# Kernel optimization log

Measured on AMD Instinct MI355X. Metric: run time of the kernel, lower is better.

## Reference

```python
import jax, jax.numpy as jnp
import numpy as np

V, D, H, L, FF, C = 32000, 512, 8, 3, 2048, 6
B, S = 32, 1024


def setup_inputs() -> dict:
    key = jax.random.key(0)
    ks = jax.random.split(key, 8)
    tokens = jax.random.randint(ks[0], (B, S), 0, V, dtype=jnp.int32)
    emb = jax.random.normal(ks[1], (V, D), dtype=jnp.float32) * 0.02
    qkv_w = jax.random.normal(ks[2], (L, D, 3 * D), dtype=jnp.float32) * (D ** -0.5)
    qkv_b = jnp.zeros((L, 3 * D), dtype=jnp.float32)
    fc_w = jax.random.normal(ks[3], (L, D, D), dtype=jnp.float32) * (D ** -0.5)
    fc_b = jnp.zeros((L, D), dtype=jnp.float32)
    gamma = jnp.ones((D,), dtype=jnp.float32)
    beta = jnp.zeros((D,), dtype=jnp.float32)
    fc1_w = jax.random.normal(ks[4], (D, FF), dtype=jnp.float32) * (D ** -0.5)
    fc1_b = jnp.zeros((FF,), dtype=jnp.float32)
    fc2_w = jax.random.normal(ks[5], (FF, C), dtype=jnp.float32) * (FF ** -0.5)
    fc2_b = jnp.zeros((C,), dtype=jnp.float32)
    return dict(tokens=tokens, emb=emb, qkv_w=qkv_w, qkv_b=qkv_b, fc_w=fc_w,
                fc_b=fc_b, gamma=gamma, beta=beta, fc1_w=fc1_w, fc1_b=fc1_b,
                fc2_w=fc2_w, fc2_b=fc2_b)


def _sinusoidal_pe(seq_len, dim):
    pos = jnp.arange(seq_len, dtype=jnp.float32)[:, None]
    div = jnp.exp(jnp.arange(0, dim, 2).astype(jnp.float32) * (-np.log(10000.0) / dim))
    pe = jnp.zeros((seq_len, dim), dtype=jnp.float32)
    pe = pe.at[:, 0::2].set(jnp.sin(pos * div))
    pe = pe.at[:, 1::2].set(jnp.cos(pos * div))
    return pe


def reference(tokens, emb, qkv_w, qkv_b, fc_w, fc_b, gamma, beta, fc1_w, fc1_b, fc2_w, fc2_b):
    b, s = tokens.shape
    dh = D // H
    scale = dh ** -0.5

    def layernorm(y):
        m = y.mean(-1, keepdims=True)
        v = ((y - m) ** 2).mean(-1, keepdims=True)
        return (y - m) * jax.lax.rsqrt(v + 1e-5) * gamma + beta

    x = emb[tokens] + _sinusoidal_pe(s, D)[None]  # [B,S,D]
    for l in range(L):
        qkv = (x @ qkv_w[l] + qkv_b[l]).reshape(b, s, H, 3, dh)
        q = qkv[..., 0, :].transpose(0, 2, 1, 3)  # [B,H,S,dh]
        k = qkv[..., 1, :].transpose(0, 2, 1, 3)
        v = qkv[..., 2, :].transpose(0, 2, 1, 3)
        attn = jax.nn.softmax(jnp.einsum('bhqd,bhkd->bhqk', q, k) * scale, axis=-1)
        o = jnp.einsum('bhqk,bhkd->bhqd', attn, v).transpose(0, 2, 1, 3).reshape(b, s, D)
        o = o @ fc_w[l] + fc_b[l]
        x = layernorm(o + x)
    pooled = x.mean(axis=1)  # [B,D]
    h = jax.nn.relu(pooled @ fc1_w + fc1_b)  # dropout is identity at inference
    return h @ fc2_w + fc2_b
```

## Files before the change

### kernel.cpp

```cpp
#include <hip/hip_runtime.h>
#include <cmath>

#define BS_TOK 32768
#define DMODEL 512
#define NHEAD 8
#define DHEAD 64
#define NLAYER 3
#define FFDIM 2048
#define NCLS 6
#define BATCH 32
#define SEQ 1024
#define QKVW 1536

typedef short short8 __attribute__((ext_vector_type(8)));
typedef float float4v __attribute__((ext_vector_type(4)));
#define MFMA_BF16 __builtin_amdgcn_mfma_f32_16x16x32_bf16
#define QSCALE 0.18033688011112042f

__device__ __forceinline__ unsigned short f2bf(float x) {
    return (unsigned short)((__float_as_uint(x) + 0x8000u) >> 16);
}

__global__ __launch_bounds__(128) void embed_pe_kernel(const int* __restrict__ tokens,
                                                       const float* __restrict__ emb,
                                                       float* __restrict__ X,
                                                       unsigned short* __restrict__ Xb) {
    int t = blockIdx.x;
    int pos = t & (SEQ - 1);
    int tok = tokens[t];
    int d0 = threadIdx.x * 4;
    float4 e = *(const float4*)(emb + (size_t)tok * DMODEL + d0);
    const float c = -9.210340371976184f / 512.0f;
    float div0 = expf((float)d0 * c);
    float div1 = expf((float)(d0 + 2) * c);
    float a0 = (float)pos * div0;
    float a1 = (float)pos * div1;
    e.x += sinf(a0); e.y += cosf(a0);
    e.z += sinf(a1); e.w += cosf(a1);
    *(float4*)(X + (size_t)t * DMODEL + d0) = e;
    *(ushort4*)(Xb + (size_t)t * DMODEL + d0) =
        make_ushort4(f2bf(e.x), f2bf(e.y), f2bf(e.z), f2bf(e.w));
}

__global__ __launch_bounds__(256) void transcvt_kernel(const float* __restrict__ in,
                                                       unsigned short* __restrict__ out,
                                                       int R, int C) {
    __shared__ float t[32][33];
    size_t base = (size_t)blockIdx.z * R * C;
    int c0 = blockIdx.x * 32, r0 = blockIdx.y * 32;
    int tx = threadIdx.x & 31, ty = threadIdx.x >> 5;
#pragma unroll
    for (int i = 0; i < 4; i++)
        t[ty + i * 8][tx] = in[base + (size_t)(r0 + ty + i * 8) * C + c0 + tx];
    __syncthreads();
#pragma unroll
    for (int i = 0; i < 4; i++)
        out[base + (size_t)(c0 + ty + i * 8) * R + r0 + tx] = f2bf(t[tx][ty + i * 8]);
}

__global__ __launch_bounds__(256) void transcvt_qkv_kernel(const float* __restrict__ in,
                                                           unsigned short* __restrict__ out) {
    __shared__ float t[32][33];
    int l = blockIdx.z;
    int n0 = blockIdx.x * 32, r0 = blockIdx.y * 32;
    int seg = n0 >> 9, nn = n0 & 511, h = nn >> 6, d0 = nn & 63;
    int c0 = h * 192 + seg * 64 + d0;
    float s = (seg == 0) ? QSCALE : 1.f;
    const float* inp = in + (size_t)l * DMODEL * QKVW;
    unsigned short* op = out + (size_t)l * QKVW * DMODEL;
    int tx = threadIdx.x & 31, ty = threadIdx.x >> 5;
#pragma unroll
    for (int i = 0; i < 4; i++)
        t[ty + i * 8][tx] = inp[(size_t)(r0 + ty + i * 8) * QKVW + c0 + tx];
    __syncthreads();
#pragma unroll
    for (int i = 0; i < 4; i++)
        op[(size_t)(n0 + ty + i * 8) * DMODEL + r0 + tx] = f2bf(t[tx][ty + i * 8] * s);
}

__global__ __launch_bounds__(256) void permbias_kernel(const float* __restrict__ qkv_b,
                                                       float* __restrict__ pb) {
    int i = blockIdx.x * 256 + threadIdx.x;
    int l = i / QKVW, n = i - l * QKVW;
    int seg = n >> 9, nn = n & 511, h = nn >> 6, d = nn & 63;
    float s = (seg == 0) ? QSCALE : 1.f;
    pb[i] = qkv_b[l * QKVW + h * 192 + seg * 64 + d] * s;
}

__global__ __launch_bounds__(256) void gemm_qkv_kernel(const unsigned short* __restrict__ A,
                                                       const unsigned short* __restrict__ Bt,
                                                       const float* __restrict__ pb,
                                                       unsigned short* __restrict__ QKc,
                                                       unsigned short* __restrict__ Vt,
                                                       int M) {
    __shared__ unsigned short As[128 * 40];
    __shared__ unsigned short Bs[128 * 40];
    int bm = blockIdx.y * 128, bn = blockIdx.x * 128;
    int tid = threadIdx.x;
    int w = tid >> 6, lane = tid & 63, l15 = lane & 15, quad = lane >> 4;
    int wm = (w & 1) * 64, wn = (w >> 1) * 64;

    float4v acc[4][4];
    float4v z = {0.f, 0.f, 0.f, 0.f};
#pragma unroll
    for (int i = 0; i < 4; i++)
#pragma unroll
        for (int j = 0; j < 4; j++) acc[i][j] = z;

    int r0 = tid >> 2, o0 = (tid & 3) * 8;
    int r1 = (tid + 256) >> 2, o1 = (tid & 3) * 8;

    for (int k0 = 0; k0 < DMODEL; k0 += 32) {
        __syncthreads();
        *(short8*)&As[r0 * 40 + o0] = *(const short8*)(A + (size_t)(bm + r0) * DMODEL + k0 + o0);
        *(short8*)&As[r1 * 40 + o1] = *(const short8*)(A + (size_t)(bm + r1) * DMODEL + k0 + o1);
        *(short8*)&Bs[r0 * 40 + o0] = *(const short8*)(Bt + (size_t)(bn + r0) * DMODEL + k0 + o0);
        *(short8*)&Bs[r1 * 40 + o1] = *(const short8*)(Bt + (size_t)(bn + r1) * DMODEL + k0 + o1);
        __syncthreads();
        short8 af[4], bf[4];
#pragma unroll
        for (int i = 0; i < 4; i++)
            af[i] = *(short8*)&As[(wm + i * 16 + l15) * 40 + quad * 8];
#pragma unroll
        for (int j = 0; j < 4; j++)
            bf[j] = *(short8*)&Bs[(wn + j * 16 + l15) * 40 + quad * 8];
#pragma unroll
        for (int i = 0; i < 4; i++)
#pragma unroll
            for (int j = 0; j < 4; j++)
                acc[i][j] = MFMA_BF16(af[i], bf[j], acc[i][j], 0, 0, 0);
    }

    float bj[4];
#pragma unroll
    for (int j = 0; j < 4; j++) bj[j] = pb[bn + wn + j * 16 + l15];

    if (bn < 1024) {
#pragma unroll
        for (int i = 0; i < 4; i++)
#pragma unroll
            for (int r = 0; r < 4; r++) {
                size_t row = (size_t)(bm + wm + i * 16 + quad * 4 + r);
#pragma unroll
                for (int j = 0; j < 4; j++)
                    QKc[row * 1024 + bn + wn + j * 16 + l15] = f2bf(acc[i][j][r] + bj[j]);
            }
    } else {
        int bl = bm >> 10;
        int sbase = (bm & 1023) + wm;
#pragma unroll
        for (int j = 0; j < 4; j++) {
            int colp = bn - 1024 + wn + j * 16 + l15;
            int h = colp >> 6, d = colp & 63;
            unsigned short* vb = Vt + ((size_t)(bl * 8 + h) * 64 + d) * 1024 + sbase;
#pragma unroll
            for (int i = 0; i < 4; i++) {
                ushort4 v4 = make_ushort4(f2bf(acc[i][j][0] + bj[j]),
                                          f2bf(acc[i][j][1] + bj[j]),
                                          f2bf(acc[i][j][2] + bj[j]),
                                          f2bf(acc[i][j][3] + bj[j]));
                *(ushort4*)(vb + i * 16 + quad * 4) = v4;
            }
        }
    }
}

__global__ __launch_bounds__(256, 2) void attn_kernel(const unsigned short* __restrict__ QKc,
                                                      const unsigned short* __restrict__ Vt,
                                                      unsigned short* __restrict__ O) {
    __shared__ unsigned short Ks[64 * 72];
    __shared__ unsigned short Vts[64 * 72];
    __shared__ unsigned short Ps[4 * 64 * 72];
    int bh = blockIdx.x;
    int b = bh >> 3, h = bh & 7;
    int q0 = blockIdx.y * 256;
    int tid = threadIdx.x;
    int w = tid >> 6, lane = tid & 63, l15 = lane & 15, quad = lane >> 4;
    unsigned short* Psb = &Ps[w * 64 * 72];
    const unsigned short* Kg = QKc + (size_t)b * SEQ * 1024 + 512 + h * 64;
    const unsigned short* Vg = Vt + (size_t)bh * 64 * 1024;

    short8 qf[4][2];
#pragma unroll
    for (int nt = 0; nt < 4; nt++) {
        const unsigned short* qb =
            QKc + (size_t)(b * SEQ + q0 + w * 64 + nt * 16 + l15) * 1024 + h * 64;
        qf[nt][0] = *(const short8*)(qb + quad * 8);
        qf[nt][1] = *(const short8*)(qb + 32 + quad * 8);
    }

    float lsum[4] = {0.f, 0.f, 0.f, 0.f};
    float4v accO[4][4];
    float4v z = {0.f, 0.f, 0.f, 0.f};
#pragma unroll
    for (int dt = 0; dt < 4; dt++)
#pragma unroll
        for (int nt = 0; nt < 4; nt++) accO[dt][nt] = z;

    for (int jt = 0; jt < SEQ / 64; jt++) {
        __syncthreads();
#pragma unroll
        for (int cc = 0; cc < 2; cc++) {
            int c = tid + cc * 256;
            int r = c >> 3, o = (c & 7) * 8;
            *(short8*)&Ks[r * 72 + o] = *(const short8*)(Kg + (size_t)(jt * 64 + r) * 1024 + o);
            *(short8*)&Vts[r * 72 + o] = *(const short8*)(Vg + (size_t)r * 1024 + jt * 64 + o);
        }
        __syncthreads();

#pragma unroll
        for (int mt = 0; mt < 4; mt++) {
            short8 kf0 = *(short8*)&Ks[(mt * 16 + l15) * 72 + quad * 8];
            short8 kf1 = *(short8*)&Ks[(mt * 16 + l15) * 72 + 32 + quad * 8];
#pragma unroll
            for (int nt = 0; nt < 4; nt++) {
                float4v sv = MFMA_BF16(kf0, qf[nt][0], z, 0, 0, 0);
                sv = MFMA_BF16(kf1, qf[nt][1], sv, 0, 0, 0);
                float p0 = exp2f(sv[0]), p1 = exp2f(sv[1]);
                float p2 = exp2f(sv[2]), p3 = exp2f(sv[3]);
                lsum[nt] += (p0 + p1) + (p2 + p3);
                unsigned int u0 = (unsigned int)f2bf(p0) | ((unsigned int)f2bf(p1) << 16);
                unsigned int u1 = (unsigned int)f2bf(p2) | ((unsigned int)f2bf(p3) << 16);
                *(uint2*)&Psb[(nt * 16 + l15) * 72 + mt * 16 + quad * 4] = make_uint2(u0, u1);
            }
        }

#pragma unroll
        for (int kc = 0; kc < 2; kc++) {
            short8 vf[4];
#pragma unroll
            for (int dt = 0; dt < 4; dt++)
                vf[dt] = *(short8*)&Vts[(dt * 16 + l15) * 72 + kc * 32 + quad * 8];
#pragma unroll
            for (int nt = 0; nt < 4; nt++) {
                short8 pfr = *(short8*)&Psb[(nt * 16 + l15) * 72 + kc * 32 + quad * 8];
#pragma unroll
                for (int dt = 0; dt < 4; dt++)
                    accO[dt][nt] = MFMA_BF16(vf[dt], pfr, accO[dt][nt], 0, 0, 0);
            }
        }
    }

#pragma unroll
    for (int nt = 0; nt < 4; nt++) {
        float s = lsum[nt];
        s += __shfl_xor(s, 16);
        s += __shfl_xor(s, 32);
        float rinv = 1.f / s;
        size_t row = (size_t)(b * SEQ + q0 + w * 64 + nt * 16 + l15);
#pragma unroll
        for (int dt = 0; dt < 4; dt++) {
            ushort4 o4 = make_ushort4(f2bf(accO[dt][nt][0] * rinv),
                                      f2bf(accO[dt][nt][1] * rinv),
                                      f2bf(accO[dt][nt][2] * rinv),
                                      f2bf(accO[dt][nt][3] * rinv));
            *(ushort4*)(O + row * DMODEL + h * DHEAD + dt * 16 + quad * 4) = o4;
        }
    }
}

__global__ __launch_bounds__(256) void proj_ln_kernel(const unsigned short* __restrict__ A,
                                                      const unsigned short* __restrict__ Bt,
                                                      const float* __restrict__ bias,
                                                      const float* __restrict__ gamma,
                                                      const float* __restrict__ beta,
                                                      float* __restrict__ X,
                                                      unsigned short* __restrict__ Xb) {
    __shared__ unsigned short As[32 * 40];
    __shared__ unsigned short Bs[512 * 40];
    __shared__ float redS[4][32], redQ[4][32];
    int bm = blockIdx.x * 32;
    int tid = threadIdx.x;
    int w = tid >> 6, lane = tid & 63, l15 = lane & 15, quad = lane >> 4;
    int wn = w * 128;

    float4v acc[2][8];
    float4v z = {0.f, 0.f, 0.f, 0.f};
#pragma unroll
    for (int i = 0; i < 2; i++)
#pragma unroll
        for (int j = 0; j < 8; j++) acc[i][j] = z;

    for (int k0 = 0; k0 < DMODEL; k0 += 32) {
        __syncthreads();
        if (tid < 128) {
            int r = tid >> 2, o = (tid & 3) * 8;
            *(short8*)&As[r * 40 + o] = *(const short8*)(A + (size_t)(bm + r) * DMODEL + k0 + o);
        }
#pragma unroll
        for (int u = 0; u < 8; u++) {
            int c = tid + u * 256;
            int r = c >> 2, o = (c & 3) * 8;
            *(short8*)&Bs[r * 40 + o] = *(const short8*)(Bt + (size_t)r * DMODEL + k0 + o);
        }
        __syncthreads();
        short8 af[2];
#pragma unroll
        for (int i = 0; i < 2; i++)
            af[i] = *(short8*)&As[(i * 16 + l15) * 40 + quad * 8];
#pragma unroll
        for (int j = 0; j < 8; j++) {
            short8 bf = *(short8*)&Bs[(wn + j * 16 + l15) * 40 + quad * 8];
            acc[0][j] = MFMA_BF16(af[0], bf, acc[0][j], 0, 0, 0);
            acc[1][j] = MFMA_BF16(af[1], bf, acc[1][j], 0, 0, 0);
        }
    }

    float bj[8], g[8], be[8];
#pragma unroll
    for (int j = 0; j < 8; j++) {
        int col = wn + j * 16 + l15;
        bj[j] = bias[col]; g[j] = gamma[col]; be[j] = beta[col];
    }

    float o[2][4][8];
#pragma unroll
    for (int i = 0; i < 2; i++)
#pragma unroll
        for (int r = 0; r < 4; r++) {
            int lrow = i * 16 + quad * 4 + r;
            size_t row = (size_t)(bm + lrow);
            float ss = 0.f, qq = 0.f;
#pragma unroll
            for (int j = 0; j < 8; j++) {
                float v = acc[i][j][r] + bj[j] + X[row * DMODEL + wn + j * 16 + l15];
                o[i][r][j] = v; ss += v; qq += v * v;
            }
#pragma unroll
            for (int mask = 1; mask < 16; mask <<= 1) {
                ss += __shfl_xor(ss, mask);
                qq += __shfl_xor(qq, mask);
            }
            if (l15 == 0) { redS[w][lrow] = ss; redQ[w][lrow] = qq; }
        }
    __syncthreads();
#pragma unroll
    for (int i = 0; i < 2; i++)
#pragma unroll
        for (int r = 0; r < 4; r++) {
            int lrow = i * 16 + quad * 4 + r;
            float S = redS[0][lrow] + redS[1][lrow] + redS[2][lrow] + redS[3][lrow];
            float Q = redQ[0][lrow] + redQ[1][lrow] + redQ[2][lrow] + redQ[3][lrow];
            float mean = S * (1.f / 512.f);
            float var = Q * (1.f / 512.f) - mean * mean;
            float rstd = rsqrtf(var + 1e-5f);
            size_t row = (size_t)(bm + lrow);
#pragma unroll
            for (int j = 0; j < 8; j++) {
                float n = (o[i][r][j] - mean) * rstd * g[j] + be[j];
                X[row * DMODEL + wn + j * 16 + l15] = n;
                Xb[row * DMODEL + wn + j * 16 + l15] = f2bf(n);
            }
        }
}

__global__ __launch_bounds__(256) void zero_kernel(float* __restrict__ p) {
    p[blockIdx.x * 256 + threadIdx.x] = 0.f;
}
__global__ __launch_bounds__(128) void pool_kernel(const float* __restrict__ X,
                                                   float* __restrict__ pooled) {
    int b = blockIdx.x, ch = blockIdx.y;
    int d0 = threadIdx.x * 4;
    float4 acc = make_float4(0.f, 0.f, 0.f, 0.f);
    const float* base = X + (size_t)(b * SEQ + ch * 64) * DMODEL + d0;
    for (int s2 = 0; s2 < 64; s2++) {
        float4 v = *(const float4*)(base + (size_t)s2 * DMODEL);
        acc.x += v.x; acc.y += v.y; acc.z += v.z; acc.w += v.w;
    }
    atomicAdd(pooled + b * DMODEL + d0 + 0, acc.x);
    atomicAdd(pooled + b * DMODEL + d0 + 1, acc.y);
    atomicAdd(pooled + b * DMODEL + d0 + 2, acc.z);
    atomicAdd(pooled + b * DMODEL + d0 + 3, acc.w);
}

__global__ __launch_bounds__(256) void fc1_kernel(const float* __restrict__ pooled,
                                                  const float* __restrict__ fc1_w,
                                                  const float* __restrict__ fc1_b,
                                                  float* __restrict__ h) {
    __shared__ float p[DMODEL];
    int ffc = blockIdx.x, b = blockIdx.y;
    int tid = threadIdx.x;
    p[tid] = pooled[b * DMODEL + tid] * (1.f / 1024.f);
    p[tid + 256] = pooled[b * DMODEL + tid + 256] * (1.f / 1024.f);
    __syncthreads();
    int ff = ffc * 256 + tid;
    float acc = fc1_b[ff];
    for (int k = 0; k < DMODEL; k++) acc += p[k] * fc1_w[(size_t)k * FFDIM + ff];
    h[(size_t)b * FFDIM + ff] = fmaxf(acc, 0.f);
}

__global__ __launch_bounds__(256) void fc2_kernel(const float* __restrict__ h,
                                                  const float* __restrict__ fc2_w,
                                                  const float* __restrict__ fc2_b,
                                                  float* __restrict__ out) {
    __shared__ float red[NCLS][256];
    int b = blockIdx.x, tid = threadIdx.x;
    float a[NCLS];
#pragma unroll
    for (int c = 0; c < NCLS; c++) a[c] = 0.f;
    int k0 = tid * 8;
#pragma unroll
    for (int u = 0; u < 8; u++) {
        float hv = h[(size_t)b * FFDIM + k0 + u];
#pragma unroll
        for (int c = 0; c < NCLS; c++) a[c] += hv * fc2_w[(k0 + u) * NCLS + c];
    }
#pragma unroll
    for (int c = 0; c < NCLS; c++) red[c][tid] = a[c];
    __syncthreads();
    if (tid < NCLS) {
        float s = 0.f;
        for (int i = 0; i < 256; i++) s += red[tid][i];
        out[b * NCLS + tid] = s + fc2_b[tid];
    }
}

extern "C" void kernel_launch(void* const* d_in, const int* in_sizes, int n_in,
                              void* d_out, int out_size, void* d_ws, size_t ws_size,
                              hipStream_t stream) {
    const int* tokens = (const int*)d_in[0];
    const float* emb = (const float*)d_in[1];
    const float* qkv_w = (const float*)d_in[2];
    const float* qkv_b = (const float*)d_in[3];
    const float* fc_w = (const float*)d_in[4];
    const float* fc_b = (const float*)d_in[5];
    const float* gamma = (const float*)d_in[6];
    const float* beta = (const float*)d_in[7];
    const float* fc1_w = (const float*)d_in[8];
    const float* fc1_b = (const float*)d_in[9];
    const float* fc2_w = (const float*)d_in[10];
    const float* fc2_b = (const float*)d_in[11];
    float* out = (float*)d_out;

    char* p = (char*)d_ws;
    float* X = (float*)p;                         p += (size_t)BS_TOK * DMODEL * 4;
    unsigned short* Xb = (unsigned short*)p;      p += (size_t)BS_TOK * DMODEL * 2;
    float* pooled = (float*)p;                    p += (size_t)BATCH * DMODEL * 4;
    float* hbuf = (float*)p;                      p += (size_t)BATCH * FFDIM * 4;
    float* pb = (float*)p;                        p += (size_t)NLAYER * QKVW * 4;
    unsigned short* qkv_wbt = (unsigned short*)p; p += (size_t)NLAYER * QKVW * DMODEL * 2;
    unsigned short* fc_wt = (unsigned short*)p;   p += (size_t)NLAYER * DMODEL * DMODEL * 2;
    size_t fixed_bytes = (size_t)(p - (char*)d_ws);
    size_t per_batch = (size_t)SEQ * 1024 * 2 + (size_t)NHEAD * 64 * SEQ * 2
                     + (size_t)SEQ * DMODEL * 2;
    int chunkB = 1;
    for (int cb = 32; cb >= 1; cb >>= 1)
        if (fixed_bytes + (size_t)cb * per_batch <= ws_size) { chunkB = cb; break; }
    unsigned short* QKc = (unsigned short*)p;     p += (size_t)chunkB * SEQ * 1024 * 2;
    unsigned short* Vt = (unsigned short*)p;      p += (size_t)chunkB * NHEAD * 64 * SEQ * 2;
    unsigned short* Oc = (unsigned short*)p;
    int rows = chunkB * SEQ;
    int nchunks = BATCH / chunkB;

    embed_pe_kernel<<<BS_TOK, 128, 0, stream>>>(tokens, emb, X, Xb);
    permbias_kernel<<<NLAYER * QKVW / 256, 256, 0, stream>>>(qkv_b, pb);
    transcvt_qkv_kernel<<<dim3(QKVW / 32, DMODEL / 32, NLAYER), 256, 0, stream>>>(
        qkv_w, qkv_wbt);
    transcvt_kernel<<<dim3(DMODEL / 32, DMODEL / 32, NLAYER), 256, 0, stream>>>(
        fc_w, fc_wt, DMODEL, DMODEL);

    for (int l = 0; l < NLAYER; l++) {
        for (int c = 0; c < nchunks; c++) {
            unsigned short* Xbc = Xb + (size_t)c * rows * DMODEL;
            float* Xc = X + (size_t)c * rows * DMODEL;
            gemm_qkv_kernel<<<dim3(QKVW / 128, rows / 128), 256, 0, stream>>>(
                Xbc, qkv_wbt + (size_t)l * QKVW * DMODEL, pb + (size_t)l * QKVW,
                QKc, Vt, rows);
            attn_kernel<<<dim3(chunkB * NHEAD, SEQ / 256), 256, 0, stream>>>(QKc, Vt, Oc);
            proj_ln_kernel<<<rows / 32, 256, 0, stream>>>(
                Oc, fc_wt + (size_t)l * DMODEL * DMODEL, fc_b + (size_t)l * DMODEL,
                gamma, beta, Xc, Xbc);
        }
    }

    zero_kernel<<<BATCH * DMODEL / 256, 256, 0, stream>>>(pooled);
    pool_kernel<<<dim3(BATCH, 16), 128, 0, stream>>>(X, pooled);
    fc1_kernel<<<dim3(FFDIM / 256, BATCH), 256, 0, stream>>>(pooled, fc1_w, fc1_b, hbuf);
    fc2_kernel<<<BATCH, 256, 0, stream>>>(hbuf, fc2_w, fc2_b, out);
}
```

Before: 1.056 ms.

## Interleave attention QK and PV per 32-key chunk to halve P shared buffer

The attention inner loop now computes QK^T scores and softmax probabilities for 32 keys at a time and immediately consumes them in the PV MFMAs. This halves the per-wave P buffer in shared memory, and the launch bounds are raised from 2 to 4 blocks per SM to exploit the smaller LDS footprint and get higher occupancy. The bf16 packing also switches to the HIP paired conversion intrinsic with round-to-nearest-even. Asking for higher occupancy may force register spills given the large accumulator arrays.

```diff
diff --git a/kernel.cpp b/kernel.cpp
--- a/kernel.cpp
+++ b/kernel.cpp
@@ -1,4 +1,5 @@
 #include <hip/hip_runtime.h>
+#include <hip/hip_bf16.h>
 #include <cmath>
 
 #define BS_TOK 32768
@@ -19,6 +20,10 @@
 
 __device__ __forceinline__ unsigned short f2bf(float x) {
     return (unsigned short)((__float_as_uint(x) + 0x8000u) >> 16);
+}
+__device__ __forceinline__ unsigned int pkbf(float a, float b) {
+    __hip_bfloat162 h = __float22bfloat162_rn(make_float2(a, b));
+    return *(unsigned int*)&h;
 }
 
 __global__ __launch_bounds__(128) void embed_pe_kernel(const int* __restrict__ tokens,
@@ -155,28 +160,26 @@
             unsigned short* vb = Vt + ((size_t)(bl * 8 + h) * 64 + d) * 1024 + sbase;
 #pragma unroll
             for (int i = 0; i < 4; i++) {
-                ushort4 v4 = make_ushort4(f2bf(acc[i][j][0] + bj[j]),
-                                          f2bf(acc[i][j][1] + bj[j]),
-                                          f2bf(acc[i][j][2] + bj[j]),
-                                          f2bf(acc[i][j][3] + bj[j]));
-                *(ushort4*)(vb + i * 16 + quad * 4) = v4;
-            }
-        }
-    }
-}
-
-__global__ __launch_bounds__(256, 2) void attn_kernel(const unsigned short* __restrict__ QKc,
+                uint2 v4 = make_uint2(pkbf(acc[i][j][0] + bj[j], acc[i][j][1] + bj[j]),
+                                      pkbf(acc[i][j][2] + bj[j], acc[i][j][3] + bj[j]));
+                *(uint2*)(vb + i * 16 + quad * 4) = v4;
+            }
+        }
+    }
+}
+
+__global__ __launch_bounds__(256, 4) void attn_kernel(const unsigned short* __restrict__ QKc,
                                                       const unsigned short* __restrict__ Vt,
                                                       unsigned short* __restrict__ O) {
     __shared__ unsigned short Ks[64 * 72];
     __shared__ unsigned short Vts[64 * 72];
-    __shared__ unsigned short Ps[4 * 64 * 72];
+    __shared__ unsigned short Ps[4 * 64 * 36];
     int bh = blockIdx.x;
     int b = bh >> 3, h = bh & 7;
     int q0 = blockIdx.y * 256;
     int tid = threadIdx.x;
     int w = tid >> 6, lane = tid & 63, l15 = lane & 15, quad = lane >> 4;
-    unsigned short* Psb = &Ps[w * 64 * 72];
+    unsigned short* Psb = &Ps[w * 64 * 36];
     const unsigned short* Kg = QKc + (size_t)b * SEQ * 1024 + 512 + h * 64;
     const unsigned short* Vg = Vt + (size_t)bh * 64 * 1024;
 
@@ -209,31 +212,30 @@
         __syncthreads();
 
 #pragma unroll
-        for (int mt = 0; mt < 4; mt++) {
-            short8 kf0 = *(short8*)&Ks[(mt * 16 + l15) * 72 + quad * 8];
-            short8 kf1 = *(short8*)&Ks[(mt * 16 + l15) * 72 + 32 + quad * 8];
-#pragma unroll
-            for (int nt = 0; nt < 4; nt++) {
-                float4v sv = MFMA_BF16(kf0, qf[nt][0], z, 0, 0, 0);
-                sv = MFMA_BF16(kf1, qf[nt][1], sv, 0, 0, 0);
-                float p0 = exp2f(sv[0]), p1 = exp2f(sv[1]);
-                float p2 = exp2f(sv[2]), p3 = exp2f(sv[3]);
-                lsum[nt] += (p0 + p1) + (p2 + p3);
-                unsigned int u0 = (unsigned int)f2bf(p0) | ((unsigned int)f2bf(p1) << 16);
-                unsigned int u1 = (unsigned int)f2bf(p2) | ((unsigned int)f2bf(p3) << 16);
-                *(uint2*)&Psb[(nt * 16 + l15) * 72 + mt * 16 + quad * 4] = make_uint2(u0, u1);
-            }
-        }
-
-#pragma unroll
         for (int kc = 0; kc < 2; kc++) {
+#pragma unroll
+            for (int mt2 = 0; mt2 < 2; mt2++) {
+                int mt = kc * 2 + mt2;
+                short8 kf0 = *(short8*)&Ks[(mt * 16 + l15) * 72 + quad * 8];
+                short8 kf1 = *(short8*)&Ks[(mt * 16 + l15) * 72 + 32 + quad * 8];
+#pragma unroll
+                for (int nt = 0; nt < 4; nt++) {
+                    float4v sv = MFMA_BF16(kf0, qf[nt][0], z, 0, 0, 0);
+                    sv = MFMA_BF16(kf1, qf[nt][1], sv, 0, 0, 0);
+                    float p0 = exp2f(sv[0]), p1 = exp2f(sv[1]);
+                    float p2 = exp2f(sv[2]), p3 = exp2f(sv[3]);
+                    lsum[nt] += (p0 + p1) + (p2 + p3);
+                    *(uint2*)&Psb[(nt * 16 + l15) * 36 + mt2 * 16 + quad * 4] =
+                        make_uint2(pkbf(p0, p1), pkbf(p2, p3));
+                }
+            }
             short8 vf[4];
 #pragma unroll
             for (int dt = 0; dt < 4; dt++)
                 vf[dt] = *(short8*)&Vts[(dt * 16 + l15) * 72 + kc * 32 + quad * 8];
 #pragma unroll
             for (int nt = 0; nt < 4; nt++) {
-                short8 pfr = *(short8*)&Psb[(nt * 16 + l15) * 72 + kc * 32 + quad * 8];
+                short8 pfr = *(short8*)&Psb[(nt * 16 + l15) * 36 + quad * 8];
 #pragma unroll
                 for (int dt = 0; dt < 4; dt++)
                     accO[dt][nt] = MFMA_BF16(vf[dt], pfr, accO[dt][nt], 0, 0, 0);
@@ -250,11 +252,9 @@
         size_t row = (size_t)(b * SEQ + q0 + w * 64 + nt * 16 + l15);
 #pragma unroll
         for (int dt = 0; dt < 4; dt++) {
-            ushort4 o4 = make_ushort4(f2bf(accO[dt][nt][0] * rinv),
-                                      f2bf(accO[dt][nt][1] * rinv),
-                                      f2bf(accO[dt][nt][2] * rinv),
-                                      f2bf(accO[dt][nt][3] * rinv));
-            *(ushort4*)(O + row * DMODEL + h * DHEAD + dt * 16 + quad * 4) = o4;
+            uint2 o4 = make_uint2(pkbf(accO[dt][nt][0] * rinv, accO[dt][nt][1] * rinv),
+                                  pkbf(accO[dt][nt][2] * rinv, accO[dt][nt][3] * rinv));
+            *(uint2*)(O + row * DMODEL + h * DHEAD + dt * 16 + quad * 4) = o4;
         }
     }
 }
```

After: 2.620 ms. 2.48x slower.
